# Kernel tuning notes

Measured on AMD Instinct MI355X. Metric: run time of the kernel, lower is better.

Reference implementation:

```python
import jax, jax.numpy as jnp
import numpy as np

H = 8          # num_head
HD = 64        # head_dim = hidden_dim // num_head
WIN = 33       # atten_window_size (odd)
MIN_SCORE = -1e9


def setup_inputs() -> dict:
    key = jax.random.key(0)
    ks = jax.random.split(key, 12)
    B, S, D = 8, 4096, 512
    scale = 1.0 / np.sqrt(D).astype(np.float32)

    def lin_w(k):
        return jax.random.normal(k, (D, D), jnp.float32) * scale

    return {
        "query": jax.random.normal(ks[0], (B, S, D), jnp.float32),
        "key": jax.random.normal(ks[1], (B, S, D), jnp.float32),
        "value": jax.random.normal(ks[2], (B, S, D), jnp.float32),
        "mask": jax.random.randint(ks[3], (B, S), 0, 2).astype(bool),
        "Wq": lin_w(ks[4]), "bq": jax.random.normal(ks[5], (D,), jnp.float32) * 0.02,
        "Wk": lin_w(ks[6]), "bk": jax.random.normal(ks[7], (D,), jnp.float32) * 0.02,
        "Wv": lin_w(ks[8]), "bv": jax.random.normal(ks[9], (D,), jnp.float32) * 0.02,
        "Wo": lin_w(ks[10]), "bo": jax.random.normal(ks[11], (D,), jnp.float32) * 0.02,
    }


def reference(query, key, value, mask, Wq, bq, Wk, bk, Wv, bv, Wo, bo):
    B, S, D = query.shape
    half = min(WIN // 2, S // 2)

    def proj_split(x, W, b):
        # nn.Linear: x @ W.T + b; then split heads and flatten (B,H) -> B*H
        y = x @ W.T + b
        return y.reshape(B, S, H, HD).transpose(0, 2, 1, 3).reshape(B * H, S, HD)

    q = proj_split(query, Wq, bq)   # [BH, S, HD]
    k = proj_split(key, Wk, bk)
    v = proj_split(value, Wv, bv)
    # mask expanded over heads; True = masked (LocalAttention semantics)
    m = jnp.broadcast_to(mask[:, None, :], (B, H, S)).reshape(B * H, S)

    # banded scores: one [BH, S] vector per window offset (no sqrt(head_dim) scaling,
    # faithful to LocalAttention)
    scores = []
    for off in range(-half, half + 1):
        if off < 0:
            w = jnp.sum(q[:, -off:] * k[:, :off], axis=-1)
            w = jnp.where(m[:, :off], MIN_SCORE, w)
            w = jnp.pad(w, ((0, 0), (-off, 0)), constant_values=MIN_SCORE)
        elif off == 0:
            w = jnp.where(m, MIN_SCORE, jnp.sum(q * k, axis=-1))
        else:
            w = jnp.sum(q[:, :-off] * k[:, off:], axis=-1)
            w = jnp.where(m[:, off:], MIN_SCORE, w)
            w = jnp.pad(w, ((0, 0), (0, off)), constant_values=MIN_SCORE)
        scores.append(w)
    probs = jax.nn.softmax(jnp.stack(scores, axis=-1), axis=-1)  # [BH, S, 2*half+1]

    # weighted gather of values along the band (dropout=0 -> identity)
    out = jnp.zeros_like(v)
    for i, off in enumerate(range(-half, half + 1)):
        p = probs[:, :, i:i + 1]
        if off < 0:
            out = out + jnp.pad(p[:, -off:] * v[:, :off], ((0, 0), (-off, 0), (0, 0)))
        elif off == 0:
            out = out + p * v
        else:
            out = out + jnp.pad(p[:, :-off] * v[:, off:], ((0, 0), (0, off), (0, 0)))

    out = out.reshape(B, H, S, HD).transpose(0, 2, 1, 3).reshape(B, S, D)
    return out @ Wo.T + bo
```

## Files before the change

kernel.cpp:

```cpp
#include <hip/hip_runtime.h>
#include <hip/hip_bf16.h>
#include <stdint.h>

#define BB 8
#define SS 4096
#define DD 512
#define HH 8
#define HDIM 64

typedef unsigned short u16;
typedef __attribute__((ext_vector_type(4))) float f32x4;
typedef __attribute__((ext_vector_type(4))) short s16x4;
typedef __attribute__((ext_vector_type(8))) short s16x8;
typedef __attribute__((ext_vector_type(4))) unsigned int u32x4;

__device__ __forceinline__ u16 f2bf(float f) {
  uint32_t x = __builtin_bit_cast(uint32_t, f);
  x += 0x7fffu + ((x >> 16) & 1u);
  return (u16)(x >> 16);
}
__device__ __forceinline__ float bf2f(u16 u) {
  uint32_t x = (uint32_t)u << 16;
  return __builtin_bit_cast(float, x);
}
__device__ __forceinline__ uint32_t cvtpk(float a, float b) {
  uint32_t d;
  asm("v_cvt_pk_bf16_f32 %0, %1, %2" : "=v"(d) : "v"(a), "v"(b));
  return d;
}

__device__ __forceinline__ void gld_lds16(const void* g, void* l) {
  __builtin_amdgcn_global_load_lds((const __attribute__((address_space(1))) void*)g,
                                   (__attribute__((address_space(3))) void*)l, 16, 0, 0);
}

__global__ void cvt_weights(const float* __restrict__ w0, const float* __restrict__ w1,
                            const float* __restrict__ w2, const float* __restrict__ w3,
                            u16* __restrict__ out) {
  int i = blockIdx.x * blockDim.x + threadIdx.x;
  const int n = DD * DD;
  if (i < n) {
    out[i]         = f2bf(w0[i]);
    out[n + i]     = f2bf(w1[i]);
    out[2 * n + i] = f2bf(w2[i]);
    out[3 * n + i] = f2bf(w3[i]);
  }
}

__global__ void mask_unpack(const void* __restrict__ mraw, uint8_t* __restrict__ mk, int n) {
  __shared__ int bad[3];
  __shared__ int mode;
  const int t = threadIdx.x;
  if (t < 3) bad[t] = 0;
  __syncthreads();
  const uint32_t* w = (const uint32_t*)mraw;
  const uint32_t x = w[t];
  const bool w01 = (x == 0u) || (x == 1u);
  const uint32_t ob = x | (x >> 8) | (x >> 16) | (x >> 24);
  const bool u01 = ((ob & 0xFEu) == 0u);
  if (!w01) atomicAdd(&bad[0], 1);
  if (!u01) atomicAdd(&bad[1], 1);
  __syncthreads();
  if (t == 0) mode = (bad[0] == 0) ? 0 : (bad[1] == 0 ? 1 : 2);
  __syncthreads();
  const int md = mode;
  for (int i = blockIdx.x * 256 + t; i < n; i += gridDim.x * 256) {
    uint8_t v;
    if (md == 0)      v = (uint8_t)(w[i] & 1u);
    else if (md == 1) v = ((const uint8_t*)mraw)[i] ? 1 : 0;
    else              v = (w[i] != 0u) ? 1 : 0;
    mk[i] = v;
  }
}

template <typename TA, typename TC>
__global__ __launch_bounds__(256, 2)
void gemm97(const TA* __restrict__ A, const u16* __restrict__ Bw,
            const float* __restrict__ bias, TC* __restrict__ C,
            int M, int N, int K) {
  constexpr bool AF32 = (sizeof(TA) == 4);
  constexpr int ABYTES = AF32 ? 128 * 64 * 4 : 128 * 64 * 2;
  __shared__ __align__(16) char sA[ABYTES];
  __shared__ __align__(16) u16 sB[128 * 64];

  const int tid = threadIdx.x;
  const int lane = tid & 63, wv = tid >> 6;
  const int wr = (wv >> 1) * 64, wc = (wv & 1) * 64;
  const int c = lane & 15, g = lane >> 4;
  const int lid = blockIdx.x;
  const int rb = (lid >> 5) * 8 + (lid & 7);
  const int cb = (lid >> 3) & 3;
  const int col0 = cb * 128, row0 = rb * 128;

  const int srB = tid >> 3, cBc = (tid & 7) ^ ((tid >> 3) & 7);
  const u16* b_src = Bw + (size_t)(col0 + srB) * K + cBc * 8;
  const int srA = tid >> 4, cAc = (tid & 15) ^ (tid >> 4);
  const TA* a_srcF = A + (size_t)(row0 + srA) * K + cAc * 4;
  const TA* a_srcH = A + (size_t)(row0 + srB) * K + cBc * 8;

  f32x4 acc[4][4];
#pragma unroll
  for (int a = 0; a < 4; ++a)
#pragma unroll
    for (int b = 0; b < 4; ++b) acc[a][b] = (f32x4){0.f, 0.f, 0.f, 0.f};

  const int nkt = K / 64;
  for (int kt = 0; kt < nkt; ++kt) {
    __syncthreads();
    const int ko = kt * 64;
    if constexpr (AF32) {
#pragma unroll
      for (int i = 0; i < 8; ++i)
        gld_lds16(a_srcF + (size_t)i * 16 * K + ko, sA + i * 4096 + wv * 1024);
    } else {
#pragma unroll
      for (int i = 0; i < 4; ++i)
        gld_lds16(a_srcH + (size_t)i * 32 * K + ko, sA + i * 4096 + wv * 1024);
    }
#pragma unroll
    for (int i = 0; i < 4; ++i)
      gld_lds16(b_src + (size_t)i * 32 * K + ko, (char*)sB + i * 4096 + wv * 1024);
    __syncthreads();

#pragma unroll
    for (int ks = 0; ks < 2; ++ks) {
      s16x8 af[4], bq[4];
#pragma unroll
      for (int mf = 0; mf < 4; ++mf) {
        const int row = wr + mf * 16 + c;
        if constexpr (AF32) {
          const int bc = ks * 128 + g * 32;
          const f32x4 lo4 = *(const f32x4*)(sA + row * 256 + ((bc) ^ (c << 4)));
          const f32x4 hi4 = *(const f32x4*)(sA + row * 256 + ((bc + 16) ^ (c << 4)));
          const u32x4 dd = (u32x4){cvtpk(lo4[0], lo4[1]), cvtpk(lo4[2], lo4[3]),
                                   cvtpk(hi4[0], hi4[1]), cvtpk(hi4[2], hi4[3])};
          af[mf] = __builtin_bit_cast(s16x8, dd);
        } else {
          const int bc = ks * 64 + g * 16;
          af[mf] = *(const s16x8*)(sA + row * 128 + (bc ^ ((c & 7) << 4)));
        }
      }
#pragma unroll
      for (int nf = 0; nf < 4; ++nf) {
        const int row = wc + nf * 16 + c;
        const int bc = ks * 64 + g * 16;
        bq[nf] = *(const s16x8*)((char*)sB + row * 128 + (bc ^ ((c & 7) << 4)));
      }
#pragma unroll
      for (int mf = 0; mf < 4; ++mf)
#pragma unroll
        for (int nf = 0; nf < 4; ++nf)
          acc[mf][nf] = __builtin_amdgcn_mfma_f32_16x16x32_bf16(af[mf], bq[nf], acc[mf][nf], 0, 0, 0);
    }
  }

#pragma unroll
  for (int nf = 0; nf < 4; ++nf) {
    const int col = col0 + wc + nf * 16 + c;
    const float bv = bias[col];
#pragma unroll
    for (int mf = 0; mf < 4; ++mf) {
#pragma unroll
      for (int i = 0; i < 4; ++i) {
        const int row = row0 + wr + mf * 16 + g * 4 + i;
        const float v = acc[mf][nf][i] + bv;
        if constexpr (sizeof(TC) == 4) C[(size_t)row * N + col] = v;
        else                           C[(size_t)row * N + col] = (TC)f2bf(v);
      }
    }
  }
}

__device__ __forceinline__ void hilo8(const f32x4& a0, const f32x4& a1, s16x8& h, s16x8& l) {
#pragma unroll
  for (int j = 0; j < 4; ++j) {
    const float f = a0[j];
    const u16 hb = f2bf(f);
    h[j] = (short)hb;
    l[j] = (short)f2bf(f - bf2f(hb));
  }
#pragma unroll
  for (int j = 0; j < 4; ++j) {
    const float f = a1[j];
    const u16 hb = f2bf(f);
    h[4 + j] = (short)hb;
    l[4 + j] = (short)f2bf(f - bf2f(hb));
  }
}

#define ACH 4
#define VSTR 100

__global__ __launch_bounds__(256, 4)
void attn_mfma(const float* __restrict__ Qp, const float* __restrict__ Kp,
               const u16* __restrict__ Vp, const uint8_t* __restrict__ mk,
               u16* __restrict__ O) {
  __shared__ u16 sKh[96 * 72];
  __shared__ u16 sKl[96 * 68];
  __shared__ u16 sVT[64 * VSTR];
  __shared__ u16 sM[96];

  const int bh = blockIdx.x;
  const int b = bh >> 3, h = bh & 7;
  const int base0 = blockIdx.y * (64 * ACH);
  const int tid = threadIdx.x;

  const int wv = tid >> 6, lane = tid & 63;
  const int c = lane & 15, g = lane >> 4;
  const int qloc = wv * 16 + c;
  const int kb = wv * 16;

  const int krow0 = tid >> 3, kj = tid & 7;
  const int kks = kj >> 2, kg2 = kj & 3;
  const int vk0 = tid >> 3, vdg8 = tid & 7;

  f32x4 kA0[3], kA1[3];
  s16x8 vR[3];
  u16 mR = 1;
  f32x4 qn0[2], qn1[2];

  auto issue_loads = [&](int cs) {
#pragma unroll
    for (int it = 0; it < 3; ++it) {
      const int row = krow0 + it * 32;
      const int gr = cs - 16 + row;
      if (gr >= 0 && gr < SS) {
        const float* kp = Kp + ((size_t)(b * SS + gr)) * DD + h * HDIM + kks * 32 + kg2 * 4;
        kA0[it] = *(const f32x4*)kp;
        kA1[it] = *(const f32x4*)(kp + 16);
      } else {
        kA0[it] = (f32x4){0.f, 0.f, 0.f, 0.f};
        kA1[it] = (f32x4){0.f, 0.f, 0.f, 0.f};
      }
    }
#pragma unroll
    for (int it = 0; it < 3; ++it) {
      const int k = vk0 + it * 32;
      const int gr = cs - 16 + k;
      if (gr >= 0 && gr < SS)
        vR[it] = *(const s16x8*)(Vp + ((size_t)(b * SS + gr)) * DD + h * HDIM + vdg8 * 8);
      else
        vR[it] = (s16x8){0, 0, 0, 0, 0, 0, 0, 0};
    }
    if (tid < 96) {
      const int gr = cs - 16 + tid;
      mR = (gr < 0 || gr >= SS || mk[b * SS + gr]) ? 1 : 0;
    }
    const float* qp = Qp + ((size_t)(b * SS + cs + qloc)) * DD + h * HDIM;
#pragma unroll
    for (int ks = 0; ks < 2; ++ks) {
      qn0[ks] = *(const f32x4*)(qp + 32 * ks + 4 * g);
      qn1[ks] = *(const f32x4*)(qp + 32 * ks + 16 + 4 * g);
    }
  };

  auto write_stage = [&]() {
#pragma unroll
    for (int it = 0; it < 3; ++it) {
      const int row = krow0 + it * 32;
      s16x8 hh, ll;
      hilo8(kA0[it], kA1[it], hh, ll);
      *(s16x8*)&sKh[row * 72 + kj * 8] = hh;
      *(s16x4*)&sKl[row * 68 + kj * 8]     = (s16x4){ll[0], ll[1], ll[2], ll[3]};
      *(s16x4*)&sKl[row * 68 + kj * 8 + 4] = (s16x4){ll[4], ll[5], ll[6], ll[7]};
    }
#pragma unroll
    for (int it = 0; it < 3; ++it) {
      const int k = vk0 + it * 32;
#pragma unroll
      for (int i = 0; i < 8; ++i)
        sVT[(vdg8 * 8 + i) * VSTR + k] = (u16)vR[it][i];
    }
    if (tid < 96) sM[tid] = mR;
  };

  issue_loads(base0);
  write_stage();
  __syncthreads();

  for (int t = 0; t < ACH; ++t) {
    const int s0 = base0 + t * 64;
    const int qrow = s0 + qloc;

    s16x8 qh[2], qlo[2];
#pragma unroll
    for (int ks = 0; ks < 2; ++ks) hilo8(qn0[ks], qn1[ks], qh[ks], qlo[ks]);

    if (t + 1 < ACH) issue_loads(base0 + (t + 1) * 64);

    f32x4 st[3];
#pragma unroll
    for (int kt = 0; kt < 3; ++kt) st[kt] = (f32x4){0.f, 0.f, 0.f, 0.f};
    __builtin_amdgcn_s_setprio(1);
#pragma unroll
    for (int kt = 0; kt < 3; ++kt) {
      const int krow = kb + kt * 16 + c;
      const int rb72 = krow * 72;
      const int rb68 = krow * 68;
#pragma unroll
      for (int ks = 0; ks < 2; ++ks) {
        const s16x8 kh = *(const s16x8*)&sKh[rb72 + ks * 32 + g * 8];
        const s16x4 l0 = *(const s16x4*)&sKl[rb68 + ks * 32 + g * 8];
        const s16x4 l1 = *(const s16x4*)&sKl[rb68 + ks * 32 + g * 8 + 4];
        const s16x8 kl = (s16x8){l0[0], l0[1], l0[2], l0[3], l1[0], l1[1], l1[2], l1[3]};
        st[kt] = __builtin_amdgcn_mfma_f32_16x16x32_bf16(kh, qh[ks], st[kt], 0, 0, 0);
        st[kt] = __builtin_amdgcn_mfma_f32_16x16x32_bf16(kh, qlo[ks], st[kt], 0, 0, 0);
        st[kt] = __builtin_amdgcn_mfma_f32_16x16x32_bf16(kl, qh[ks], st[kt], 0, 0, 0);
      }
    }
    __builtin_amdgcn_s_setprio(0);

    float mx = -3.0e9f;
#pragma unroll
    for (int kt = 0; kt < 3; ++kt) {
#pragma unroll
      for (int i = 0; i < 4; ++i) {
        const int delta = kt * 16 + 4 * g + i - 16 - c;
        const int key = kb + kt * 16 + 4 * g + i;
        float v;
        if (delta < -16 || delta > 16) v = -2.0e9f;
        else if (sM[key])              v = -1.0e9f;
        else                           v = st[kt][i];
        st[kt][i] = v;
        mx = fmaxf(mx, v);
      }
    }
    mx = fmaxf(mx, __shfl_xor(mx, 16));
    mx = fmaxf(mx, __shfl_xor(mx, 32));
    float sum = 0.f;
#pragma unroll
    for (int kt = 0; kt < 3; ++kt) {
#pragma unroll
      for (int i = 0; i < 4; ++i) {
        const float e = __expf(st[kt][i] - mx);
        st[kt][i] = e;
        sum += e;
      }
    }
    sum += __shfl_xor(sum, 16);
    sum += __shfl_xor(sum, 32);
    const float inv = 1.f / sum;

    s16x8 ph[2];
#pragma unroll
    for (int i = 0; i < 4; ++i) {
      ph[0][i]     = (short)f2bf(st[0][i]);
      ph[0][4 + i] = (short)f2bf(st[1][i]);
      ph[1][i]     = (short)f2bf(st[2][i]);
      ph[1][4 + i] = 0;
    }

    f32x4 ot[4];
#pragma unroll
    for (int dt = 0; dt < 4; ++dt) ot[dt] = (f32x4){0.f, 0.f, 0.f, 0.f};
    __builtin_amdgcn_s_setprio(1);
#pragma unroll
    for (int dt = 0; dt < 4; ++dt) {
      const int rowb = (dt * 16 + c) * VSTR;
      const s16x4 v0 = *(const s16x4*)&sVT[rowb + kb + 4 * g];
      const s16x4 v1 = *(const s16x4*)&sVT[rowb + kb + 16 + 4 * g];
      const s16x8 vh0 = (s16x8){v0[0], v0[1], v0[2], v0[3], v1[0], v1[1], v1[2], v1[3]};
      ot[dt] = __builtin_amdgcn_mfma_f32_16x16x32_bf16(vh0, ph[0], ot[dt], 0, 0, 0);
      const s16x4 v2 = *(const s16x4*)&sVT[rowb + kb + 32 + 4 * g];
      const s16x8 vh1 = (s16x8){v2[0], v2[1], v2[2], v2[3], 0, 0, 0, 0};
      ot[dt] = __builtin_amdgcn_mfma_f32_16x16x32_bf16(vh1, ph[1], ot[dt], 0, 0, 0);
    }
    __builtin_amdgcn_s_setprio(0);

    u16* op = O + ((size_t)(b * SS + qrow)) * DD + h * HDIM;
#pragma unroll
    for (int dt = 0; dt < 4; ++dt) {
      s16x4 pk;
#pragma unroll
      for (int i = 0; i < 4; ++i) pk[i] = (short)f2bf(ot[dt][i] * inv);
      *(s16x4*)&op[dt * 16 + 4 * g] = pk;
    }

    __syncthreads();
    if (t + 1 < ACH) {
      write_stage();
      __syncthreads();
    }
  }
}

__global__ __launch_bounds__(256)
void attn_win(const u16* __restrict__ Qp, const u16* __restrict__ Kp,
              const u16* __restrict__ Vp, const uint8_t* __restrict__ mk,
              u16* __restrict__ O) {
  constexpr int KR = 96;
  __shared__ float sK[KR][HDIM];
  __shared__ float sV[KR][HDIM];
  __shared__ float sMf[KR];

  const int bh = blockIdx.x;
  const int b = bh >> 3, h = bh & 7;
  const int s0 = blockIdx.y * 64;
  const int tid = threadIdx.x;

  for (int c = tid; c < KR * 16; c += 256) {
    const int row = c >> 4, c4 = c & 15;
    const int gr = s0 - 16 + row;
    float kv[4], vv[4];
    if (gr >= 0 && gr < SS) {
      const size_t base = ((size_t)(b * SS + gr)) * DD + h * HDIM + c4 * 4;
      const s16x4 kk = *(const s16x4*)(Kp + base);
      const s16x4 vx = *(const s16x4*)(Vp + base);
#pragma unroll
      for (int i = 0; i < 4; ++i) { kv[i] = bf2f((u16)kk[i]); vv[i] = bf2f((u16)vx[i]); }
    } else {
#pragma unroll
      for (int i = 0; i < 4; ++i) { kv[i] = 0.f; vv[i] = 0.f; }
    }
#pragma unroll
    for (int i = 0; i < 4; ++i) {
      const int d = c4 * 4 + i;
      const int pd = (d & 15) * 4 + (d >> 4);
      sK[row][pd] = kv[i];
      sV[row][pd] = vv[i];
    }
  }
  for (int r = tid; r < KR; r += 256) {
    const int gr = s0 - 16 + r;
    sMf[r] = (gr < 0 || gr >= SS || mk[b * SS + gr]) ? 1.f : 0.f;
  }
  __syncthreads();

  const int wv = tid >> 6, lane = tid & 63;
  const int g = lane >> 4, d16 = lane & 15;

  for (int rr = 0; rr < 16; rr += 4) {
    const int lr = wv * 16 + rr + g;
    const int srow = s0 + lr;
    const u16* qp = Qp + ((size_t)(b * SS + srow)) * DD + h * HDIM;
    float q0 = bf2f(qp[d16]), q1 = bf2f(qp[d16 + 16]), q2 = bf2f(qp[d16 + 32]), q3 = bf2f(qp[d16 + 48]);
    float sc[33];
#pragma unroll
    for (int o = 0; o < 33; ++o) {
      const f32x4 kk = *(const f32x4*)&sK[lr + o][d16 * 4];
      float p = q0 * kk[0] + q1 * kk[1] + q2 * kk[2] + q3 * kk[3];
      p += __shfl_xor(p, 1);
      p += __shfl_xor(p, 2);
      p += __shfl_xor(p, 4);
      p += __shfl_xor(p, 8);
      sc[o] = (sMf[lr + o] != 0.f) ? -1.0e9f : p;
    }
    float mx = sc[0];
#pragma unroll
    for (int o = 1; o < 33; ++o) mx = fmaxf(mx, sc[o]);
    float sum = 0.f;
#pragma unroll
    for (int o = 0; o < 33; ++o) { const float e = __expf(sc[o] - mx); sc[o] = e; sum += e; }
    const float inv = 1.f / sum;
    f32x4 acc = (f32x4){0.f, 0.f, 0.f, 0.f};
#pragma unroll
    for (int o = 0; o < 33; ++o) {
      const f32x4 vx = *(const f32x4*)&sV[lr + o][d16 * 4];
      acc += (sc[o] * inv) * vx;
    }
    u16* op = O + ((size_t)(b * SS + srow)) * DD + h * HDIM;
    op[d16]      = f2bf(acc[0]);
    op[d16 + 16] = f2bf(acc[1]);
    op[d16 + 32] = f2bf(acc[2]);
    op[d16 + 48] = f2bf(acc[3]);
  }
}

extern "C" void kernel_launch(void* const* d_in, const int* in_sizes, int n_in,
                              void* d_out, int out_size, void* d_ws, size_t ws_size,
                              hipStream_t stream) {
  const float* query = (const float*)d_in[0];
  const float* key   = (const float*)d_in[1];
  const float* value = (const float*)d_in[2];
  const void*  mraw  = d_in[3];
  const float* Wq = (const float*)d_in[4];
  const float* bq = (const float*)d_in[5];
  const float* Wk = (const float*)d_in[6];
  const float* bk = (const float*)d_in[7];
  const float* Wv = (const float*)d_in[8];
  const float* bv = (const float*)d_in[9];
  const float* Wo = (const float*)d_in[10];
  const float* bo = (const float*)d_in[11];

  const int M = BB * SS, N = DD, K = DD;

  char* ws = (char*)d_ws;
  size_t off = 0;
  auto carve = [&](size_t bytes) -> char* {
    char* p = ws + off;
    off = (off + bytes + 255) & ~(size_t)255;
    return p;
  };
  u16* wAll   = (u16*)carve((size_t)4 * DD * DD * sizeof(u16));
  uint8_t* mk = (uint8_t*)carve((size_t)BB * SS);

  const size_t qk_f32 = (size_t)M * DD * 4;
  const size_t v_b16  = (size_t)M * DD * 2;
  const bool f32p = (off + 2 * qk_f32 + 2 * v_b16 + 1024) <= ws_size;

  cvt_weights<<<(DD * DD + 255) / 256, 256, 0, stream>>>(Wq, Wk, Wv, Wo, wAll);
  mask_unpack<<<16, 256, 0, stream>>>(mraw, mk, BB * SS);

  const dim3 gg((M / 128) * (N / 128));
  const dim3 ga(BB * HH, SS / (64 * ACH));

  if (f32p) {
    float* Qf = (float*)carve(qk_f32);
    float* Kf = (float*)carve(qk_f32);
    u16*   Vb = (u16*)carve(v_b16);
    u16*   AO = (u16*)carve(v_b16);
    gemm97<float, float><<<gg, 256, 0, stream>>>(query, wAll,               bq, Qf, M, N, K);
    gemm97<float, float><<<gg, 256, 0, stream>>>(key,   wAll + DD * DD,     bk, Kf, M, N, K);
    gemm97<float, u16><<<gg, 256, 0, stream>>>(value, wAll + 2 * DD * DD, bv, Vb, M, N, K);
    attn_mfma<<<ga, 256, 0, stream>>>(Qf, Kf, Vb, mk, AO);
    gemm97<u16, float><<<gg, 256, 0, stream>>>(AO, wAll + 3 * DD * DD, bo, (float*)d_out, M, N, K);
  } else {
    const dim3 ga1(BB * HH, SS / 64);
    u16* Qb = (u16*)carve(v_b16);
    u16* Kb = (u16*)carve(v_b16);
    u16* Vb = (u16*)carve(v_b16);
    u16* AO = (u16*)carve(v_b16);
    gemm97<float, u16><<<gg, 256, 0, stream>>>(query, wAll,               bq, Qb, M, N, K);
    gemm97<float, u16><<<gg, 256, 0, stream>>>(key,   wAll + DD * DD,     bk, Kb, M, N, K);
    gemm97<float, u16><<<gg, 256, 0, stream>>>(value, wAll + 2 * DD * DD, bv, Vb, M, N, K);
    attn_win<<<ga1, 256, 0, stream>>>(Qb, Kb, Vb, mk, AO);
    gemm97<u16, float><<<gg, 256, 0, stream>>>(AO, wAll + 3 * DD * DD, bo, (float*)d_out, M, N, K);
  }
}
```

Baseline: 224.4 us.

## Pre-convert activations to bf16 and double-buffer GEMM LDS tiles

Adds a standalone kernel that converts each fp32 input (query, key, value) to bf16 in a shared scratch buffer before its projection GEMM. The GEMM becomes bf16-only with two LDS buffers, so the next K-tile is prefetched while MFMAs run on the current one. This is meant to cut the fp32 LDS traffic and in-loop conversion and to hide load latency. The cost is an extra full read and write pass over each input, plus doubled LDS use that may lower occupancy.

```diff
diff --git a/kernel.cpp b/kernel.cpp
--- a/kernel.cpp
+++ b/kernel.cpp
@@ -23,15 +23,25 @@
   uint32_t x = (uint32_t)u << 16;
   return __builtin_bit_cast(float, x);
 }
-__device__ __forceinline__ uint32_t cvtpk(float a, float b) {
-  uint32_t d;
-  asm("v_cvt_pk_bf16_f32 %0, %1, %2" : "=v"(d) : "v"(a), "v"(b));
-  return d;
-}
 
 __device__ __forceinline__ void gld_lds16(const void* g, void* l) {
   __builtin_amdgcn_global_load_lds((const __attribute__((address_space(1))) void*)g,
                                    (__attribute__((address_space(3))) void*)l, 16, 0, 0);
+}
+
+__global__ void cvt_f32_bf16(const float* __restrict__ in, u16* __restrict__ out, int n8) {
+  int i = blockIdx.x * blockDim.x + threadIdx.x;
+  const int stride = gridDim.x * blockDim.x;
+  for (; i < n8; i += stride) {
+    const f32x4 a0 = *(const f32x4*)(in + (size_t)i * 8);
+    const f32x4 a1 = *(const f32x4*)(in + (size_t)i * 8 + 4);
+    s16x8 pk;
+#pragma unroll
+    for (int j = 0; j < 4; ++j) pk[j] = (short)f2bf(a0[j]);
+#pragma unroll
+    for (int j = 0; j < 4; ++j) pk[4 + j] = (short)f2bf(a1[j]);
+    *(s16x8*)(out + (size_t)i * 8) = pk;
+  }
 }
 
 __global__ void cvt_weights(const float* __restrict__ w0, const float* __restrict__ w1,
@@ -73,15 +83,13 @@
   }
 }
 
-template <typename TA, typename TC>
+template <typename TC>
 __global__ __launch_bounds__(256, 2)
-void gemm97(const TA* __restrict__ A, const u16* __restrict__ Bw,
-            const float* __restrict__ bias, TC* __restrict__ C,
-            int M, int N, int K) {
-  constexpr bool AF32 = (sizeof(TA) == 4);
-  constexpr int ABYTES = AF32 ? 128 * 64 * 4 : 128 * 64 * 2;
-  __shared__ __align__(16) char sA[ABYTES];
-  __shared__ __align__(16) u16 sB[128 * 64];
+void gemm_db(const u16* __restrict__ A, const u16* __restrict__ Bw,
+             const float* __restrict__ bias, TC* __restrict__ C,
+             int M, int N, int K) {
+  __shared__ __align__(16) u16 sA[2][128 * 64];
+  __shared__ __align__(16) u16 sB[2][128 * 64];
 
   const int tid = threadIdx.x;
   const int lane = tid & 63, wv = tid >> 6;
@@ -93,10 +101,17 @@
   const int col0 = cb * 128, row0 = rb * 128;
 
   const int srB = tid >> 3, cBc = (tid & 7) ^ ((tid >> 3) & 7);
+  const u16* a_src = A + (size_t)(row0 + srB) * K + cBc * 8;
   const u16* b_src = Bw + (size_t)(col0 + srB) * K + cBc * 8;
-  const int srA = tid >> 4, cAc = (tid & 15) ^ (tid >> 4);
-  const TA* a_srcF = A + (size_t)(row0 + srA) * K + cAc * 4;
-  const TA* a_srcH = A + (size_t)(row0 + srB) * K + cBc * 8;
+
+  auto stage = [&](int buf, int ko) {
+#pragma unroll
+    for (int i = 0; i < 4; ++i)
+      gld_lds16(a_src + (size_t)i * 32 * K + ko, (char*)sA[buf] + i * 4096 + wv * 1024);
+#pragma unroll
+    for (int i = 0; i < 4; ++i)
+      gld_lds16(b_src + (size_t)i * 32 * K + ko, (char*)sB[buf] + i * 4096 + wv * 1024);
+  };
 
   f32x4 acc[4][4];
 #pragma unroll
@@ -105,22 +120,11 @@
     for (int b = 0; b < 4; ++b) acc[a][b] = (f32x4){0.f, 0.f, 0.f, 0.f};
 
   const int nkt = K / 64;
+  stage(0, 0);
+  __syncthreads();
+  int cur = 0;
   for (int kt = 0; kt < nkt; ++kt) {
-    __syncthreads();
-    const int ko = kt * 64;
-    if constexpr (AF32) {
-#pragma unroll
-      for (int i = 0; i < 8; ++i)
-        gld_lds16(a_srcF + (size_t)i * 16 * K + ko, sA + i * 4096 + wv * 1024);
-    } else {
-#pragma unroll
-      for (int i = 0; i < 4; ++i)
-        gld_lds16(a_srcH + (size_t)i * 32 * K + ko, sA + i * 4096 + wv * 1024);
-    }
-#pragma unroll
-    for (int i = 0; i < 4; ++i)
-      gld_lds16(b_src + (size_t)i * 32 * K + ko, (char*)sB + i * 4096 + wv * 1024);
-    __syncthreads();
+    if (kt + 1 < nkt) stage(cur ^ 1, (kt + 1) * 64);
 
 #pragma unroll
     for (int ks = 0; ks < 2; ++ks) {
@@ -128,23 +132,12 @@
 #pragma unroll
       for (int mf = 0; mf < 4; ++mf) {
         const int row = wr + mf * 16 + c;
-        if constexpr (AF32) {
-          const int bc = ks * 128 + g * 32;
-          const f32x4 lo4 = *(const f32x4*)(sA + row * 256 + ((bc) ^ (c << 4)));
-          const f32x4 hi4 = *(const f32x4*)(sA + row * 256 + ((bc + 16) ^ (c << 4)));
-          const u32x4 dd = (u32x4){cvtpk(lo4[0], lo4[1]), cvtpk(lo4[2], lo4[3]),
-                                   cvtpk(hi4[0], hi4[1]), cvtpk(hi4[2], hi4[3])};
-          af[mf] = __builtin_bit_cast(s16x8, dd);
-        } else {
-          const int bc = ks * 64 + g * 16;
-          af[mf] = *(const s16x8*)(sA + row * 128 + (bc ^ ((c & 7) << 4)));
-        }
+        af[mf] = *(const s16x8*)&sA[cur][row * 64 + (((ks * 4 + g) ^ (c & 7)) * 8)];
       }
 #pragma unroll
       for (int nf = 0; nf < 4; ++nf) {
         const int row = wc + nf * 16 + c;
-        const int bc = ks * 64 + g * 16;
-        bq[nf] = *(const s16x8*)((char*)sB + row * 128 + (bc ^ ((c & 7) << 4)));
+        bq[nf] = *(const s16x8*)&sB[cur][row * 64 + (((ks * 4 + g) ^ (c & 7)) * 8)];
       }
 #pragma unroll
       for (int mf = 0; mf < 4; ++mf)
@@ -152,6 +145,8 @@
         for (int nf = 0; nf < 4; ++nf)
           acc[mf][nf] = __builtin_amdgcn_mfma_f32_16x16x32_bf16(af[mf], bq[nf], acc[mf][nf], 0, 0, 0);
     }
+    __syncthreads();
+    cur ^= 1;
   }
 
 #pragma unroll
@@ -493,37 +488,45 @@
   };
   u16* wAll   = (u16*)carve((size_t)4 * DD * DD * sizeof(u16));
   uint8_t* mk = (uint8_t*)carve((size_t)BB * SS);
+  u16* Xb     = (u16*)carve((size_t)M * DD * 2);
 
   const size_t qk_f32 = (size_t)M * DD * 4;
   const size_t v_b16  = (size_t)M * DD * 2;
-  const bool f32p = (off + 2 * qk_f32 + 2 * v_b16 + 1024) <= ws_size;
+  const bool f32p = (off + 2 * qk_f32 + v_b16 + 1024) <= ws_size;
 
   cvt_weights<<<(DD * DD + 255) / 256, 256, 0, stream>>>(Wq, Wk, Wv, Wo, wAll);
   mask_unpack<<<16, 256, 0, stream>>>(mraw, mk, BB * SS);
 
+  const int n8 = M * DD / 8;
+  const dim3 gc(2048);
   const dim3 gg((M / 128) * (N / 128));
   const dim3 ga(BB * HH, SS / (64 * ACH));
+  u16* AO = Xb;
 
   if (f32p) {
     float* Qf = (float*)carve(qk_f32);
     float* Kf = (float*)carve(qk_f32);
     u16*   Vb = (u16*)carve(v_b16);
-    u16*   AO = (u16*)carve(v_b16);
-    gemm97<float, float><<<gg, 256, 0, stream>>>(query, wAll,               bq, Qf, M, N, K);
-    gemm97<float, float><<<gg, 256, 0, stream>>>(key,   wAll + DD * DD,     bk, Kf, M, N, K);
-    gemm97<float, u16><<<gg, 256, 0, stream>>>(value, wAll + 2 * DD * DD, bv, Vb, M, N, K);
+    cvt_f32_bf16<<<gc, 256, 0, stream>>>(query, Xb, n8);
+    gemm_db<float><<<gg, 256, 0, stream>>>(Xb, wAll,               bq, Qf, M, N, K);
+    cvt_f32_bf16<<<gc, 256, 0, stream>>>(key, Xb, n8);
+    gemm_db<float><<<gg, 256, 0, stream>>>(Xb, wAll + DD * DD,     bk, Kf, M, N, K);
+    cvt_f32_bf16<<<gc, 256, 0, stream>>>(value, Xb, n8);
+    gemm_db<u16><<<gg, 256, 0, stream>>>(Xb, wAll + 2 * DD * DD, bv, Vb, M, N, K);
     attn_mfma<<<ga, 256, 0, stream>>>(Qf, Kf, Vb, mk, AO);
-    gemm97<u16, float><<<gg, 256, 0, stream>>>(AO, wAll + 3 * DD * DD, bo, (float*)d_out, M, N, K);
+    gemm_db<float><<<gg, 256, 0, stream>>>(AO, wAll + 3 * DD * DD, bo, (float*)d_out, M, N, K);
   } else {
     const dim3 ga1(BB * HH, SS / 64);
     u16* Qb = (u16*)carve(v_b16);
     u16* Kb = (u16*)carve(v_b16);
     u16* Vb = (u16*)carve(v_b16);
-    u16* AO = (u16*)carve(v_b16);
-    gemm97<float, u16><<<gg, 256, 0, stream>>>(query, wAll,               bq, Qb, M, N, K);
-    gemm97<float, u16><<<gg, 256, 0, stream>>>(key,   wAll + DD * DD,     bk, Kb, M, N, K);
-    gemm97<float, u16><<<gg, 256, 0, stream>>>(value, wAll + 2 * DD * DD, bv, Vb, M, N, K);
+    cvt_f32_bf16<<<gc, 256, 0, stream>>>(query, Xb, n8);
+    gemm_db<u16><<<gg, 256, 0, stream>>>(Xb, wAll,               bq, Qb, M, N, K);
+    cvt_f32_bf16<<<gc, 256, 0, stream>>>(key, Xb, n8);
+    gemm_db<u16><<<gg, 256, 0, stream>>>(Xb, wAll + DD * DD,     bk, Kb, M, N, K);
+    cvt_f32_bf16<<<gc, 256, 0, stream>>>(value, Xb, n8);
+    gemm_db<u16><<<gg, 256, 0, stream>>>(Xb, wAll + 2 * DD * DD, bv, Vb, M, N, K);
     attn_win<<<ga1, 256, 0, stream>>>(Qb, Kb, Vb, mk, AO);
-    gemm97<u16, float><<<gg, 256, 0, stream>>>(AO, wAll + 3 * DD * DD, bo, (float*)d_out, M, N, K);
-  }
-}
+    gemm_db<float><<<gg, 256, 0, stream>>>(AO, wAll + 3 * DD * DD, bo, (float*)d_out, M, N, K);
+  }
+}
```

Result: slower. 242.3 us (+8.0%).
